# Kernel tuning notes

Measured on AMD Instinct MI355X. Metric: run time of the kernel, lower is better.

Reference implementation:

```python
import jax, jax.numpy as jnp
import numpy as np

B, S, D, N = 4, 2048, 1024, 256
BLK = 16                       # b = sqrt(state_dim)
DFF = int(8 / 3 * D)           # 2730, SwiGLU default
EPS = 1e-6


def setup_inputs() -> dict:
    key = jax.random.key(0)
    ks = jax.random.split(key, 12)
    rn = lambda k, shape, s=0.02: jax.random.normal(k, shape, jnp.float32) * s
    return {
        "x": jax.random.normal(ks[0], (B, S, D), jnp.float32),
        "L_skew": rn(ks[1], (BLK, BLK, BLK), 0.01),
        "R_skew": rn(ks[2], (BLK, BLK, BLK), 0.01),
        "Wg": rn(ks[3], (2 * BLK, D)), "bg": jnp.zeros((2 * BLK,), jnp.float32),
        "WB": rn(ks[4], (N, D)), "bB": jnp.zeros((N,), jnp.float32),
        "WC": rn(ks[5], (D, N)), "bC": jnp.zeros((D,), jnp.float32),
        "norm1_w": jnp.ones((D,), jnp.float32),
        "norm2_w": jnp.ones((D,), jnp.float32),
        "w1": rn(ks[6], (DFF, D)), "w2": rn(ks[7], (DFF, D)), "w3": rn(ks[8], (D, DFF)),
    }


def cayley(skew):
    # Q = (I + A)^{-1} (I - A), A skew-symmetric -> Q orthogonal
    A = skew - jnp.swapaxes(skew, -2, -1)
    I = jnp.eye(A.shape[-1], dtype=A.dtype)
    return jnp.linalg.solve(I + A, I - A)


def rmsnorm(x, w):
    rms = jnp.sqrt(jnp.mean(x * x, axis=-1, keepdims=True) + EPS)
    return w * x / rms


def reference(x, L_skew, R_skew, Wg, bg, WB, bB, WC, bC, norm1_w, norm2_w, w1, w2, w3):
    xs = rmsnorm(x, norm1_w)
    L_Q = cayley(L_skew)  # (b,b,b)
    R_Q = cayley(R_skew)

    # per-step input-dependent quantities, computed in one batched GEMM each
    gates = jax.nn.sigmoid(jnp.einsum('bsd,gd->bsg', xs, Wg) + bg)  # (B,S,2b)
    alpha, beta = gates[..., :BLK], gates[..., BLK:]
    Bx = jnp.einsum('bsd,nd->bsn', xs, WB) + bB                      # (B,S,N)

    def step(h, inp):
        a, be, bx = inp                       # (B,b),(B,b),(B,N)
        hb = h.reshape(-1, BLK, BLK)          # block view of state
        hr = jnp.einsum('cij,Bcj->Bci', R_Q, hb) * be[:, :, None]
        hp = jnp.swapaxes(hr, 1, 2)           # perm P_b (block transpose)
        hl = jnp.einsum('cij,Bcj->Bci', L_Q, hp) * a[:, :, None]
        h_new = jnp.swapaxes(hl, 1, 2).reshape(-1, N) + bx  # inv perm + B x_t
        return h_new, h_new

    h0 = jnp.zeros((x.shape[0], N), x.dtype)
    _, hs = jax.lax.scan(
        step, h0,
        (alpha.transpose(1, 0, 2), beta.transpose(1, 0, 2), Bx.transpose(1, 0, 2)))
    hs = hs.transpose(1, 0, 2)                                       # (B,S,N)
    y = jnp.einsum('bsn,dn->bsd', hs, WC) + bC

    x = x + y
    xn = rmsnorm(x, norm2_w)
    ff = jnp.einsum('bsf,df->bsd',
                    jax.nn.silu(jnp.einsum('bsd,fd->bsf', xn, w1)) *
                    jnp.einsum('bsd,fd->bsf', xn, w2), w3)
    return x + ff
```

## Files before the change

### kernel.cpp

```cpp
#include <hip/hip_runtime.h>
#include <hip/hip_bf16.h>

#define S_LEN  2048
#define BATCH  4
#define DIM    1024
#define NSTATE 256
#define DFF    2730
#define DFFP   2752
#define DFQ    2816
#define NROWS  (BATCH * S_LEN)
#define LC     16
#define WARM   32
#define NBG    384

#define PB_CAYLEY 0
#define PB_WBG    (PB_CAYLEY + 32)
#define PB_WC     (PB_WBG + NBG)
#define PB_W1     (PB_WC + 256)
#define PB_W2     (PB_W1 + DFQ)
#define PB_W3     (PB_W2 + DFQ)
#define PB_RMS    (PB_W3 + 11 * DIM)
#define PB_TOTAL  (PB_RMS + NROWS)

typedef __attribute__((ext_vector_type(8))) short bf16x8;
typedef __attribute__((ext_vector_type(4))) float f32x4;

__device__ __forceinline__ float bf2f(ushort u) {
    return __uint_as_float(((unsigned int)u) << 16);
}
__device__ __forceinline__ ushort f2bf(float f) {
    unsigned int u = __float_as_uint(f);
    u += 0x7fffu + ((u >> 16) & 1u);
    return (ushort)(u >> 16);
}

__device__ __forceinline__ void gld_lds16(const ushort* g, ushort* l) {
    __builtin_amdgcn_global_load_lds(
        (const __attribute__((address_space(1))) unsigned int*)g,
        (__attribute__((address_space(3))) unsigned int*)l,
        16, 0, 0);
}

__global__ __launch_bounds__(256) void prep_kernel(
    const float* __restrict__ Lsk, const float* __restrict__ Rsk,
    float* __restrict__ QL, float* __restrict__ QR,
    const float* __restrict__ WB, const float* __restrict__ Wg,
    ushort* __restrict__ WBGb,
    const float* __restrict__ WC, ushort* __restrict__ WCb,
    const float* __restrict__ w1, ushort* __restrict__ w1p,
    const float* __restrict__ w2, ushort* __restrict__ w2p,
    const float* __restrict__ w3, ushort* __restrict__ w3p,
    const float* __restrict__ x, const float* __restrict__ n1w,
    ushort* __restrict__ xs)
{
    const int bid = blockIdx.x, t = threadIdx.x;

    if (bid < PB_WBG) {
        __shared__ float Ms[16][17];
        __shared__ float Rh[16][17];
        const int m = bid;
        const float* src = (m < 16) ? (Lsk + m * 256) : (Rsk + (m - 16) * 256);
        const int i = t >> 4, j = t & 15;
        float a = src[i * 16 + j] - src[j * 16 + i];
        float eye = (i == j) ? 1.f : 0.f;
        Ms[i][j] = eye + a;
        Rh[i][j] = eye - a;
        __syncthreads();
        for (int k = 0; k < 16; ++k) {
            float f = Ms[i][k] / Ms[k][k];
            __syncthreads();
            if (i != k) {
                Ms[i][j] -= f * Ms[k][j];
                Rh[i][j] -= f * Rh[k][j];
            }
            __syncthreads();
        }
        float q = Rh[i][j] / Ms[i][i];
        float* dst = (m < 16) ? (QL + m * 256) : (QR + (m - 16) * 256);
        dst[i * 16 + j] = q;
    } else if (bid < PB_WC) {
        const int row = bid - PB_WBG;
        ushort4 o = {0, 0, 0, 0};
        const float* src = nullptr;
        if (row < NSTATE) src = WB + (size_t)row * DIM;
        else if (row < NSTATE + 32) src = Wg + (size_t)(row - NSTATE) * DIM;
        if (src) {
            float4 v = *(const float4*)(src + t * 4);
            o.x = f2bf(v.x); o.y = f2bf(v.y); o.z = f2bf(v.z); o.w = f2bf(v.w);
        }
        *(ushort4*)(WBGb + (size_t)row * DIM + t * 4) = o;
    } else if (bid < PB_W1) {
        const int i = (bid - PB_WC) * 256 + t;
        float4 v = *(const float4*)(WC + i * 4);
        ushort4 o;
        o.x = f2bf(v.x); o.y = f2bf(v.y); o.z = f2bf(v.z); o.w = f2bf(v.w);
        *(ushort4*)(WCb + i * 4) = o;
    } else if (bid < PB_W2) {
        const int row = bid - PB_W1;
        ushort4 o = {0, 0, 0, 0};
        if (row < DFF) {
            float4 v = *(const float4*)(w1 + (size_t)row * DIM + t * 4);
            o.x = f2bf(v.x); o.y = f2bf(v.y); o.z = f2bf(v.z); o.w = f2bf(v.w);
        }
        *(ushort4*)(w1p + (size_t)row * DIM + t * 4) = o;
    } else if (bid < PB_W3) {
        const int row = bid - PB_W2;
        ushort4 o = {0, 0, 0, 0};
        if (row < DFF) {
            float4 v = *(const float4*)(w2 + (size_t)row * DIM + t * 4);
            o.x = f2bf(v.x); o.y = f2bf(v.y); o.z = f2bf(v.z); o.w = f2bf(v.w);
        }
        *(ushort4*)(w2p + (size_t)row * DIM + t * 4) = o;
    } else if (bid < PB_RMS) {
        const int lid = bid - PB_W3;
        const int row = lid / 11, cb = lid % 11;
        const int col = cb * 256 + t;
        if (col < DFFP) {
            ushort v = 0;
            if (col < DFF) v = f2bf(w3[(size_t)row * DFF + col]);
            w3p[(size_t)row * DFFP + col] = v;
        }
    } else {
        __shared__ float part[4];
        __shared__ float invs;
        const int row = bid - PB_RMS;
        float4 xv = *(const float4*)(x + (size_t)row * DIM + t * 4);
        float ss = xv.x * xv.x + xv.y * xv.y + xv.z * xv.z + xv.w * xv.w;
        for (int off = 32; off > 0; off >>= 1) ss += __shfl_down(ss, off, 64);
        if ((t & 63) == 0) part[t >> 6] = ss;
        __syncthreads();
        if (t == 0) {
            float tot = part[0] + part[1] + part[2] + part[3];
            invs = 1.f / sqrtf(tot / (float)DIM + 1e-6f);
        }
        __syncthreads();
        float inv = invs;
        float4 wv = *(const float4*)(n1w + t * 4);
        ushort4 ov;
        ov.x = f2bf(wv.x * xv.x * inv);
        ov.y = f2bf(wv.y * xv.y * inv);
        ov.z = f2bf(wv.z * xv.z * inv);
        ov.w = f2bf(wv.w * xv.w * inv);
        *(ushort4*)(xs + (size_t)row * DIM + t * 4) = ov;
    }
}

__global__ __launch_bounds__(256) void rms_kernel(
    const float* __restrict__ xin, const float* __restrict__ nw,
    ushort* __restrict__ xo)
{
    __shared__ float part[4];
    __shared__ float invs;
    const int row = blockIdx.x, t = threadIdx.x;
    float4 xv = *(const float4*)(xin + (size_t)row * DIM + t * 4);
    float ss = xv.x * xv.x + xv.y * xv.y + xv.z * xv.z + xv.w * xv.w;
    for (int off = 32; off > 0; off >>= 1) ss += __shfl_down(ss, off, 64);
    if ((t & 63) == 0) part[t >> 6] = ss;
    __syncthreads();
    if (t == 0) {
        float tot = part[0] + part[1] + part[2] + part[3];
        invs = 1.f / sqrtf(tot / (float)DIM + 1e-6f);
    }
    __syncthreads();
    float inv = invs;
    float4 wv = *(const float4*)(nw + t * 4);
    ushort4 ov;
    ov.x = f2bf(wv.x * xv.x * inv);
    ov.y = f2bf(wv.y * xv.y * inv);
    ov.z = f2bf(wv.z * xv.z * inv);
    ov.w = f2bf(wv.w * xv.w * inv);
    *(ushort4*)(xo + (size_t)row * DIM + t * 4) = ov;
}

__global__ __launch_bounds__(256) void scan_win_kernel(
    const float* __restrict__ QL, const float* __restrict__ QR,
    const float* __restrict__ gates, const float* __restrict__ Bx,
    ushort* __restrict__ hs)
{
    __shared__ float Hs[256];
    __shared__ float Us[2][256];
    const int chunk = blockIdx.x, b = blockIdx.y, t = threadIdx.x;
    const int hi = t >> 4, lo = t & 15;
    float Rrow[16], Lrow[16];
    #pragma unroll
    for (int k = 0; k < 16; ++k) {
        Rrow[k] = QR[hi * 256 + lo * 16 + k];
        Lrow[k] = QL[lo * 256 + hi * 16 + k];
    }
    Hs[t] = 0.f;
    __syncthreads();
    const int wstart = chunk * LC;
    const int s0 = (wstart >= WARM) ? (wstart - WARM) : 0;
    const int send = wstart + LC;
    const float* gb = gates + (size_t)b * S_LEN * 32;
    const float* xb = Bx + (size_t)b * S_LEN * NSTATE;
    ushort* hb = hs + (size_t)b * S_LEN * NSTATE;
    float beta  = gb[s0 * 32 + 16 + hi];
    float alpha = gb[s0 * 32 + lo];
    float bx    = xb[s0 * NSTATE + t];
    int q = 0;
    for (int s = s0; s < send; ++s) {
        float betaN = 0.f, alphaN = 0.f, bxN = 0.f;
        if (s + 1 < send) {
            betaN  = gb[(s + 1) * 32 + 16 + hi];
            alphaN = gb[(s + 1) * 32 + lo];
            bxN    = xb[(s + 1) * NSTATE + t];
        }
        float acc = 0.f;
        #pragma unroll
        for (int k = 0; k < 16; ++k) acc += Rrow[k] * Hs[hi * 16 + k];
        Us[q][t] = beta * acc;
        asm volatile("s_waitcnt lgkmcnt(0)" ::: "memory");
        __builtin_amdgcn_s_barrier();
        asm volatile("" ::: "memory");
        float acc2 = 0.f;
        #pragma unroll
        for (int k = 0; k < 16; ++k) acc2 += Lrow[k] * Us[q][k * 16 + lo];
        float h = alpha * acc2 + bx;
        Hs[t] = h;
        if (s >= wstart) hb[s * NSTATE + t] = f2bf(h);
        beta = betaN; alpha = alphaN; bx = bxN;
        q ^= 1;
    }
}

__global__ __launch_bounds__(256) void gemm_async(
    const ushort* __restrict__ A, int lda,
    const ushort* __restrict__ B, int ldb,
    int K, int ldc,
    const float* __restrict__ bias,
    const float* __restrict__ resF,
    float* __restrict__ outF)
{
    __shared__ ushort As[128 * 64];
    __shared__ ushort Bs[128 * 64];
    const int tid = threadIdx.x;
    const int m0 = blockIdx.y * 128, n0 = blockIdx.x * 128;
    const int w = tid >> 6, lane = tid & 63;
    const int wm = (w >> 1) * 64, wn = (w & 1) * 64;
    const int lr = lane & 15, quad = lane >> 4;
    const int rx = lr & 7;
    f32x4 acc[4][4];
    #pragma unroll
    for (int i = 0; i < 4; ++i)
        #pragma unroll
        for (int j = 0; j < 4; ++j) acc[i][j] = (f32x4){0.f, 0.f, 0.f, 0.f};
    const int srow = tid >> 3;
    const int scol = (((tid & 7) ^ (srow & 7)) * 8);
    const ushort* ga = A + (size_t)(m0 + srow) * lda + scol;
    const ushort* gb = B + (size_t)(n0 + srow) * ldb + scol;
    for (int kt = 0; kt < K; kt += 64) {
        #pragma unroll
        for (int p = 0; p < 4; ++p) {
            gld_lds16(ga + (size_t)(p * 32) * lda + kt, &As[p * 2048 + tid * 8]);
            gld_lds16(gb + (size_t)(p * 32) * ldb + kt, &Bs[p * 2048 + tid * 8]);
        }
        __syncthreads();
        #pragma unroll
        for (int s = 0; s < 2; ++s) {
            const int cg = ((s * 4 + quad) ^ rx) * 8;
            bf16x8 af[4], bfr[4];
            #pragma unroll
            for (int f = 0; f < 4; ++f) {
                af[f]  = *(const bf16x8*)&As[(wm + f * 16 + lr) * 64 + cg];
                bfr[f] = *(const bf16x8*)&Bs[(wn + f * 16 + lr) * 64 + cg];
            }
            #pragma unroll
            for (int i = 0; i < 4; ++i)
                #pragma unroll
                for (int j = 0; j < 4; ++j)
                    acc[i][j] = __builtin_amdgcn_mfma_f32_16x16x32_bf16(
                        af[i], bfr[j], acc[i][j], 0, 0, 0);
        }
        __syncthreads();
    }
    #pragma unroll
    for (int i = 0; i < 4; ++i) {
        int row = m0 + wm + i * 16 + quad * 4;
        #pragma unroll
        for (int j = 0; j < 4; ++j) {
            int col = n0 + wn + j * 16 + lr;
            float bv = bias ? bias[col] : 0.f;
            #pragma unroll
            for (int r = 0; r < 4; ++r) {
                size_t idx = (size_t)(row + r) * ldc + col;
                float v = acc[i][j][r] + bv;
                if (resF) v += resF[idx];
                outF[idx] = v;
            }
        }
    }
}

__global__ __launch_bounds__(256) void gemm_bxg(
    const ushort* __restrict__ A,
    const ushort* __restrict__ WBG,
    const float* __restrict__ bB, const float* __restrict__ bg,
    float* __restrict__ Bx, float* __restrict__ gates)
{
    __shared__ ushort As[128 * 64];
    __shared__ ushort Bs[128 * 64];
    const int tid = threadIdx.x;
    const int m0 = blockIdx.y * 128, n0 = blockIdx.x * 128;
    const int w = tid >> 6, lane = tid & 63;
    const int wm = (w >> 1) * 64, wn = (w & 1) * 64;
    const int lr = lane & 15, quad = lane >> 4;
    const int rx = lr & 7;
    f32x4 acc[4][4];
    #pragma unroll
    for (int i = 0; i < 4; ++i)
        #pragma unroll
        for (int j = 0; j < 4; ++j) acc[i][j] = (f32x4){0.f, 0.f, 0.f, 0.f};
    const int srow = tid >> 3;
    const int scol = (((tid & 7) ^ (srow & 7)) * 8);
    const ushort* ga = A   + (size_t)(m0 + srow) * DIM + scol;
    const ushort* gb = WBG + (size_t)(n0 + srow) * DIM + scol;
    for (int kt = 0; kt < DIM; kt += 64) {
        #pragma unroll
        for (int p = 0; p < 4; ++p) {
            gld_lds16(ga + (size_t)(p * 32) * DIM + kt, &As[p * 2048 + tid * 8]);
            gld_lds16(gb + (size_t)(p * 32) * DIM + kt, &Bs[p * 2048 + tid * 8]);
        }
        __syncthreads();
        #pragma unroll
        for (int s = 0; s < 2; ++s) {
            const int cg = ((s * 4 + quad) ^ rx) * 8;
            bf16x8 af[4], bfr[4];
            #pragma unroll
            for (int f = 0; f < 4; ++f) {
                af[f]  = *(const bf16x8*)&As[(wm + f * 16 + lr) * 64 + cg];
                bfr[f] = *(const bf16x8*)&Bs[(wn + f * 16 + lr) * 64 + cg];
            }
            #pragma unroll
            for (int i = 0; i < 4; ++i)
                #pragma unroll
                for (int j = 0; j < 4; ++j)
                    acc[i][j] = __builtin_amdgcn_mfma_f32_16x16x32_bf16(
                        af[i], bfr[j], acc[i][j], 0, 0, 0);
        }
        __syncthreads();
    }
    #pragma unroll
    for (int i = 0; i < 4; ++i) {
        int row = m0 + wm + i * 16 + quad * 4;
        #pragma unroll
        for (int j = 0; j < 4; ++j) {
            int col = n0 + wn + j * 16 + lr;
            #pragma unroll
            for (int r = 0; r < 4; ++r) {
                float v = acc[i][j][r];
                if (col < NSTATE) {
                    Bx[(size_t)(row + r) * NSTATE + col] = v + bB[col];
                } else if (col < NSTATE + 32) {
                    int g = col - NSTATE;
                    gates[(size_t)(row + r) * 32 + g] =
                        1.f / (1.f + expf(-(v + bg[g])));
                }
            }
        }
    }
}

__global__ __launch_bounds__(256, 2) void ffn_gemm(
    const ushort* __restrict__ A,
    const ushort* __restrict__ B1,
    const ushort* __restrict__ B2,
    ushort* __restrict__ pb)
{
    __shared__ ushort As [128 * 64];
    __shared__ ushort B1s[128 * 64];
    __shared__ ushort B2s[128 * 64];
    const int tid = threadIdx.x;
    const int m0 = blockIdx.y * 128, n0 = blockIdx.x * 128;
    const int w = tid >> 6, lane = tid & 63;
    const int wm = (w >> 1) * 64, wn = (w & 1) * 64;
    const int lr = lane & 15, quad = lane >> 4;
    const int rx = lr & 7;
    f32x4 acc1[4][4], acc2[4][4];
    #pragma unroll
    for (int i = 0; i < 4; ++i)
        #pragma unroll
        for (int j = 0; j < 4; ++j) {
            acc1[i][j] = (f32x4){0.f, 0.f, 0.f, 0.f};
            acc2[i][j] = (f32x4){0.f, 0.f, 0.f, 0.f};
        }
    const int srow = tid >> 3;
    const int scol = (((tid & 7) ^ (srow & 7)) * 8);
    const ushort* ga  = A  + (size_t)(m0 + srow) * DIM + scol;
    const ushort* gb1 = B1 + (size_t)(n0 + srow) * DIM + scol;
    const ushort* gb2 = B2 + (size_t)(n0 + srow) * DIM + scol;
    for (int kt = 0; kt < DIM; kt += 64) {
        #pragma unroll
        for (int p = 0; p < 4; ++p) {
            gld_lds16(ga  + (size_t)(p * 32) * DIM + kt, &As [p * 2048 + tid * 8]);
            gld_lds16(gb1 + (size_t)(p * 32) * DIM + kt, &B1s[p * 2048 + tid * 8]);
            gld_lds16(gb2 + (size_t)(p * 32) * DIM + kt, &B2s[p * 2048 + tid * 8]);
        }
        __syncthreads();
        #pragma unroll
        for (int s = 0; s < 2; ++s) {
            const int cg = ((s * 4 + quad) ^ rx) * 8;
            bf16x8 af[4], b1f[4], b2f[4];
            #pragma unroll
            for (int f = 0; f < 4; ++f) {
                af[f]  = *(const bf16x8*)&As [(wm + f * 16 + lr) * 64 + cg];
                b1f[f] = *(const bf16x8*)&B1s[(wn + f * 16 + lr) * 64 + cg];
                b2f[f] = *(const bf16x8*)&B2s[(wn + f * 16 + lr) * 64 + cg];
            }
            #pragma unroll
            for (int i = 0; i < 4; ++i)
                #pragma unroll
                for (int j = 0; j < 4; ++j) {
                    acc1[i][j] = __builtin_amdgcn_mfma_f32_16x16x32_bf16(
                        af[i], b1f[j], acc1[i][j], 0, 0, 0);
                    acc2[i][j] = __builtin_amdgcn_mfma_f32_16x16x32_bf16(
                        af[i], b2f[j], acc2[i][j], 0, 0, 0);
                }
        }
        __syncthreads();
    }
    #pragma unroll
    for (int i = 0; i < 4; ++i) {
        int row = m0 + wm + i * 16 + quad * 4;
        #pragma unroll
        for (int j = 0; j < 4; ++j) {
            int col = n0 + wn + j * 16 + lr;
            if (col < DFFP) {
                #pragma unroll
                for (int r = 0; r < 4; ++r) {
                    float v1 = acc1[i][j][r];
                    float v2 = acc2[i][j][r];
                    float p = v1 / (1.f + expf(-v1)) * v2;
                    pb[(size_t)(row + r) * DFFP + col] = f2bf(p);
                }
            }
        }
    }
}

extern "C" void kernel_launch(void* const* d_in, const int* in_sizes, int n_in,
                              void* d_out, int out_size, void* d_ws, size_t ws_size,
                              hipStream_t stream) {
    const float* x   = (const float*)d_in[0];
    const float* Lsk = (const float*)d_in[1];
    const float* Rsk = (const float*)d_in[2];
    const float* Wg  = (const float*)d_in[3];
    const float* bg  = (const float*)d_in[4];
    const float* WB  = (const float*)d_in[5];
    const float* bB  = (const float*)d_in[6];
    const float* WC  = (const float*)d_in[7];
    const float* bC  = (const float*)d_in[8];
    const float* n1w = (const float*)d_in[9];
    const float* n2w = (const float*)d_in[10];
    const float* w1  = (const float*)d_in[11];
    const float* w2  = (const float*)d_in[12];
    const float* w3  = (const float*)d_in[13];
    float* out = (float*)d_out;

    char* wp = (char*)d_ws;
    auto carve = [&](size_t bytes) -> char* {
        char* p = wp;
        wp += (bytes + 255) & ~(size_t)255;
        return p;
    };
    float*  QL    = (float*)carve(16 * 256 * 4);
    float*  QR    = (float*)carve(16 * 256 * 4);
    ushort* WBGb  = (ushort*)carve((size_t)NBG * DIM * 2);
    ushort* WCb   = (ushort*)carve((size_t)DIM * NSTATE * 2);
    ushort* w1p   = (ushort*)carve((size_t)DFQ * DIM * 2);
    ushort* w2p   = (ushort*)carve((size_t)DFQ * DIM * 2);
    ushort* w3p   = (ushort*)carve((size_t)DIM * DFFP * 2);
    ushort* xs    = (ushort*)carve((size_t)NROWS * DIM * 2);
    float*  x2    = (float*)carve((size_t)NROWS * DIM * 4);
    ushort* pb    = (ushort*)carve((size_t)NROWS * DFFP * 2);
    char*   scr   = carve((size_t)16 << 20);
    float*  gates = (float*)scr;
    float*  Bx    = (float*)(scr + (1 << 21));
    ushort* hs    = (ushort*)(scr + (11u << 20));
    ushort* xn    = xs;

    prep_kernel<<<PB_TOTAL, 256, 0, stream>>>(
        Lsk, Rsk, QL, QR, WB, Wg, WBGb, WC, WCb,
        w1, w1p, w2, w2p, w3, w3p, x, n1w, xs);
    gemm_bxg<<<dim3(3, 64), 256, 0, stream>>>(xs, WBGb, bB, bg, Bx, gates);
    scan_win_kernel<<<dim3(S_LEN / LC, BATCH), 256, 0, stream>>>(QL, QR, gates, Bx, hs);
    gemm_async<<<dim3(8, 64), 256, 0, stream>>>(hs, NSTATE, WCb, NSTATE, NSTATE, DIM,
                                                bC, x, x2);
    rms_kernel<<<NROWS, 256, 0, stream>>>(x2, n2w, xn);
    ffn_gemm<<<dim3(DFQ / 128, 64), 256, 0, stream>>>(xn, w1p, w2p, pb);
    gemm_async<<<dim3(8, 64), 256, 0, stream>>>(pb, DFFP, w3p, DFFP, DFFP, DIM,
                                                nullptr, x2, out);
}
```

Before: 414.0 us.

## Fuse second RMSNorm into output-projection GEMM via last-block row counters

Removes the standalone rms_kernel launch. The C-projection GEMM now does the RMSNorm itself: each block bumps a per-row-tile atomic counter, and the last of the 8 column blocks for a 128-row tile reads the finished x2 rows back and writes the normalized bf16 xn. Counters are zeroed by an extra block in the prep kernel. The scan chunk length LC is also halved, which doubles the number of scan blocks at the cost of more warm-up recompute per chunk. The fused tail serializes the norm onto one block per row tile and depends on the threadfence ordering being correct.

```diff
diff --git a/kernel.cpp b/kernel.cpp
--- a/kernel.cpp
+++ b/kernel.cpp
@@ -9,7 +9,7 @@
 #define DFFP   2752
 #define DFQ    2816
 #define NROWS  (BATCH * S_LEN)
-#define LC     16
+#define LC     8
 #define WARM   32
 #define NBG    384
 
@@ -20,7 +20,8 @@
 #define PB_W2     (PB_W1 + DFQ)
 #define PB_W3     (PB_W2 + DFQ)
 #define PB_RMS    (PB_W3 + 11 * DIM)
-#define PB_TOTAL  (PB_RMS + NROWS)
+#define PB_ZC     (PB_RMS + NROWS)
+#define PB_TOTAL  (PB_ZC + 1)
 
 typedef __attribute__((ext_vector_type(8))) short bf16x8;
 typedef __attribute__((ext_vector_type(4))) float f32x4;
@@ -51,7 +52,7 @@
     const float* __restrict__ w2, ushort* __restrict__ w2p,
     const float* __restrict__ w3, ushort* __restrict__ w3p,
     const float* __restrict__ x, const float* __restrict__ n1w,
-    ushort* __restrict__ xs)
+    ushort* __restrict__ xs, int* __restrict__ cnt)
 {
     const int bid = blockIdx.x, t = threadIdx.x;
 
@@ -120,7 +121,7 @@
             if (col < DFF) v = f2bf(w3[(size_t)row * DFF + col]);
             w3p[(size_t)row * DFFP + col] = v;
         }
-    } else {
+    } else if (bid < PB_ZC) {
         __shared__ float part[4];
         __shared__ float invs;
         const int row = bid - PB_RMS;
@@ -142,34 +143,9 @@
         ov.z = f2bf(wv.z * xv.z * inv);
         ov.w = f2bf(wv.w * xv.w * inv);
         *(ushort4*)(xs + (size_t)row * DIM + t * 4) = ov;
-    }
-}
-
-__global__ __launch_bounds__(256) void rms_kernel(
-    const float* __restrict__ xin, const float* __restrict__ nw,
-    ushort* __restrict__ xo)
-{
-    __shared__ float part[4];
-    __shared__ float invs;
-    const int row = blockIdx.x, t = threadIdx.x;
-    float4 xv = *(const float4*)(xin + (size_t)row * DIM + t * 4);
-    float ss = xv.x * xv.x + xv.y * xv.y + xv.z * xv.z + xv.w * xv.w;
-    for (int off = 32; off > 0; off >>= 1) ss += __shfl_down(ss, off, 64);
-    if ((t & 63) == 0) part[t >> 6] = ss;
-    __syncthreads();
-    if (t == 0) {
-        float tot = part[0] + part[1] + part[2] + part[3];
-        invs = 1.f / sqrtf(tot / (float)DIM + 1e-6f);
-    }
-    __syncthreads();
-    float inv = invs;
-    float4 wv = *(const float4*)(nw + t * 4);
-    ushort4 ov;
-    ov.x = f2bf(wv.x * xv.x * inv);
-    ov.y = f2bf(wv.y * xv.y * inv);
-    ov.z = f2bf(wv.z * xv.z * inv);
-    ov.w = f2bf(wv.w * xv.w * inv);
-    *(ushort4*)(xo + (size_t)row * DIM + t * 4) = ov;
+    } else {
+        if (t < 64) cnt[t] = 0;
+    }
 }
 
 __global__ __launch_bounds__(256) void scan_win_kernel(
@@ -230,7 +206,10 @@
     int K, int ldc,
     const float* __restrict__ bias,
     const float* __restrict__ resF,
-    float* __restrict__ outF)
+    float* __restrict__ outF,
+    int* __restrict__ cnt,
+    const float* __restrict__ nw,
+    ushort* __restrict__ xo)
 {
     __shared__ ushort As[128 * 64];
     __shared__ ushort Bs[128 * 64];
@@ -287,6 +266,42 @@
                 float v = acc[i][j][r] + bv;
                 if (resF) v += resF[idx];
                 outF[idx] = v;
+            }
+        }
+    }
+    if (cnt) {
+        __threadfence();
+        __shared__ int oldc;
+        if (tid == 0) oldc = atomicAdd(&cnt[blockIdx.y], 1);
+        __syncthreads();
+        if (oldc == (int)gridDim.x - 1) {
+            __threadfence();
+            const int wv = tid >> 6;
+            const float* base = outF + (size_t)m0 * ldc;
+            for (int r = wv * 32; r < wv * 32 + 32; ++r) {
+                const float* rp = base + (size_t)r * ldc;
+                float4 v[4];
+                float ss = 0.f;
+                #pragma unroll
+                for (int c = 0; c < 4; ++c) {
+                    v[c] = *(const float4*)(rp + lane * 4 + c * 256);
+                    ss += v[c].x * v[c].x + v[c].y * v[c].y
+                        + v[c].z * v[c].z + v[c].w * v[c].w;
+                }
+                for (int off = 32; off > 0; off >>= 1)
+                    ss += __shfl_down(ss, off, 64);
+                ss = __shfl(ss, 0, 64);
+                float inv = 1.f / sqrtf(ss / (float)DIM + 1e-6f);
+                #pragma unroll
+                for (int c = 0; c < 4; ++c) {
+                    float4 wv4 = *(const float4*)(nw + lane * 4 + c * 256);
+                    ushort4 o;
+                    o.x = f2bf(wv4.x * v[c].x * inv);
+                    o.y = f2bf(wv4.y * v[c].y * inv);
+                    o.z = f2bf(wv4.z * v[c].z * inv);
+                    o.w = f2bf(wv4.w * v[c].w * inv);
+                    *(ushort4*)(xo + (size_t)(m0 + r) * DIM + lane * 4 + c * 256) = o;
+                }
             }
         }
     }
@@ -465,6 +480,7 @@
     };
     float*  QL    = (float*)carve(16 * 256 * 4);
     float*  QR    = (float*)carve(16 * 256 * 4);
+    int*    cnt   = (int*)carve(64 * 4);
     ushort* WBGb  = (ushort*)carve((size_t)NBG * DIM * 2);
     ushort* WCb   = (ushort*)carve((size_t)DIM * NSTATE * 2);
     ushort* w1p   = (ushort*)carve((size_t)DFQ * DIM * 2);
@@ -481,13 +497,12 @@
 
     prep_kernel<<<PB_TOTAL, 256, 0, stream>>>(
         Lsk, Rsk, QL, QR, WB, Wg, WBGb, WC, WCb,
-        w1, w1p, w2, w2p, w3, w3p, x, n1w, xs);
+        w1, w1p, w2, w2p, w3, w3p, x, n1w, xs, cnt);
     gemm_bxg<<<dim3(3, 64), 256, 0, stream>>>(xs, WBGb, bB, bg, Bx, gates);
     scan_win_kernel<<<dim3(S_LEN / LC, BATCH), 256, 0, stream>>>(QL, QR, gates, Bx, hs);
     gemm_async<<<dim3(8, 64), 256, 0, stream>>>(hs, NSTATE, WCb, NSTATE, NSTATE, DIM,
-                                                bC, x, x2);
-    rms_kernel<<<NROWS, 256, 0, stream>>>(x2, n2w, xn);
+                                                bC, x, x2, cnt, n2w, xn);
     ffn_gemm<<<dim3(DFQ / 128, 64), 256, 0, stream>>>(xn, w1p, w2p, pb);
     gemm_async<<<dim3(8, 64), 256, 0, stream>>>(pb, DFFP, w3p, DFFP, DFFP, DIM,
-                                                nullptr, x2, out);
-}
+                                                nullptr, x2, out, nullptr, nullptr, nullptr);
+}
```

Measured after the change: 493.7 us. +19.2%, slower.
